# Kernel optimization log

Hardware: AMD Instinct MI355X
Metric: run time of the kernel (lower is better)

The kernel has to match this reference:

```python
import jax, jax.numpy as jnp
import numpy as np

ALPHA = 300.0  # attractor strength (exp variant: exp(-alpha*|dx|^gamma)*dx, gamma=2)


def setup_inputs() -> dict:
    key = jax.random.key(0)
    k0, k1, k2, k3 = jax.random.split(key, 4)
    n, c, h, w = 4, 256, 128, 128
    mlp_dim, n_attractors, n_bins = 128, 16, 64
    x = jax.random.normal(k0, (n, c, h, w), jnp.float32)
    b_prev = jax.random.uniform(k1, (n, n_bins, h, w), jnp.float32)  # bin centers
    w1 = jax.random.normal(k2, (mlp_dim, c), jnp.float32) * 0.02
    b1 = jnp.zeros((mlp_dim,), jnp.float32)
    w2 = jax.random.normal(k3, (n_attractors, mlp_dim), jnp.float32) * 0.02
    b2 = jnp.zeros((n_attractors,), jnp.float32)
    return {"x": x, "b_prev": b_prev, "w1": w1, "b1": b1, "w2": w2, "b2": b2}


def reference(x, b_prev, w1, b1, w2, b2):
    # 1x1 conv MLP head: Conv2d(c->mlp) -> ReLU -> Conv2d(mlp->n_attractors) -> Softplus
    hfeat = jax.nn.relu(jnp.einsum('nchw,oc->nohw', x, w1) + b1[None, :, None, None])
    A = jax.nn.softplus(jnp.einsum('nchw,oc->nohw', hfeat, w2) + b2[None, :, None, None])
    # b_prev interpolated to (h, w) == identity here (same spatial size)
    b_centers = b_prev
    # dx: [n, n_attractors, n_bins, h, w]
    dx = A[:, :, None, :, :] - b_centers[:, None, :, :, :]
    # exp attractor with gamma=2: exp(-alpha*dx^2) * dx, summed over attractors ('sum' kind)
    delta_c = jnp.sum(jnp.exp(-ALPHA * dx * dx) * dx, axis=1)
    b_new_centers = b_centers + delta_c
    return (b_new_centers, b_new_centers)
```

## Files before the change

### kernel.cpp

```cpp
#include <hip/hip_runtime.h>
#include <hip/hip_bf16.h>
#include <stdint.h>


#define HW 16384
#define ALPHA 300.0f

typedef short bf16x8_t __attribute__((ext_vector_type(8)));
typedef float f32x4_t __attribute__((ext_vector_type(4)));
typedef unsigned int u32x4_t __attribute__((ext_vector_type(4)));

__device__ __forceinline__ unsigned short f2bf(float f) {
  unsigned int u = __builtin_bit_cast(unsigned int, f);
  u += 0x7fffu + ((u >> 16) & 1u);
  return (unsigned short)(u >> 16);
}
__device__ __forceinline__ unsigned int pack2(float a, float b) {
  return (unsigned int)f2bf(a) | ((unsigned int)f2bf(b) << 16);
}

__global__ void zoed_prep(const float* __restrict__ w1,
                          const float* __restrict__ w2,
                          unsigned short* __restrict__ blob) {
  int i = blockIdx.x * 256 + threadIdx.x;
  if (i < 32768) {
    int o = i >> 8, c = i & 255;
    float v = w1[i];
    int idx = (c >> 5) * 4096 + o * 32 + ((((c >> 3) & 3) ^ (o & 3)) << 3) + (c & 7);
    blob[idx] = f2bf(v);
  } else {
    int i2 = i - 32768;
    int a = i2 >> 7, o = i2 & 127;
    float v = w2[i2];
    int idx = 32768 + (o >> 5) * 512 + a * 32 + ((((o >> 3) & 3) ^ (a & 3)) << 3) + (o & 7);
    blob[idx] = f2bf(v);
  }
}

__global__ __launch_bounds__(256, 4) void zoed_fused(
    const float* __restrict__ x, const float* __restrict__ bprev,
    const float* __restrict__ b1, const float* __restrict__ b2,
    const unsigned short* __restrict__ wblob, float* __restrict__ out) {
  __shared__ __align__(16) char smem[21504];

  const int t = threadIdx.x;
  const int lane = t & 63;
  const int l15 = lane & 15;
  const int quad = lane >> 4;
  const int wv = t >> 6;
  const int sw = ((quad ^ (l15 & 3)) << 4);

  const int blk = blockIdx.x;
  const int n = blk >> 8;
  const int p0 = ((blk & 255) << 6) + wv * 16;

  char* hid = smem + wv * 4096;
  char* Ab = smem + 16384 + wv * 1280;

  const float* xb = x + (size_t)(n * 256 + quad * 8) * HW + p0 + l15;

  float xr[4][8];
#pragma unroll
  for (int c = 0; c < 3; c++)
#pragma unroll
    for (int j = 0; j < 8; j++)
      xr[c][j] = xb[(size_t)(c * 32 + j) * HW];

  size_t obase = (size_t)(n * 64 + quad * 16) * HW + p0 + l15;
  const float* bp = bprev + obase;
  float bpr[16];

  f32x4_t acc[8];
#pragma unroll
  for (int i = 0; i < 8; i++) acc[i] = (f32x4_t){0.f, 0.f, 0.f, 0.f};

  const char* wb = (const char*)wblob + l15 * 64 + sw;

#pragma unroll
  for (int kb = 0; kb < 8; ++kb) {
    bf16x8_t af[8];
#pragma unroll
    for (int tm = 0; tm < 8; tm++)
      af[tm] = *(const bf16x8_t*)(wb + kb * 8192 + tm * 1024);
    if (kb < 5) {
#pragma unroll
      for (int j = 0; j < 8; j++)
        xr[(kb + 3) & 3][j] = xb[(size_t)((kb + 3) * 32 + j) * HW];
    }
    if (kb == 5) {
#pragma unroll
      for (int b = 0; b < 8; b++) bpr[b] = bp[(size_t)b * HW];
    }
    if (kb == 6) {
#pragma unroll
      for (int b = 8; b < 16; b++) bpr[b] = bp[(size_t)b * HW];
    }
    u32x4_t v = {pack2(xr[kb & 3][0], xr[kb & 3][1]),
                 pack2(xr[kb & 3][2], xr[kb & 3][3]),
                 pack2(xr[kb & 3][4], xr[kb & 3][5]),
                 pack2(xr[kb & 3][6], xr[kb & 3][7])};
    bf16x8_t bfm = __builtin_bit_cast(bf16x8_t, v);
#pragma unroll
    for (int tm = 0; tm < 8; tm++)
      acc[tm] = __builtin_amdgcn_mfma_f32_16x16x32_bf16(af[tm], bfm, acc[tm],
                                                        0, 0, 0);
  }

  bf16x8_t a2[4];
#pragma unroll
  for (int kc = 0; kc < 4; kc++)
    a2[kc] = *(const bf16x8_t*)((const char*)wblob + 65536 + kc * 1024 +
                                l15 * 64 + sw);

#pragma unroll
  for (int tm = 0; tm < 8; tm++) {
    f32x4_t b1v = *(const f32x4_t*)(b1 + tm * 16 + quad * 4);
    f32x4_t h = acc[tm] + b1v;
    h[0] = fmaxf(h[0], 0.f);
    h[1] = fmaxf(h[1], 0.f);
    h[2] = fmaxf(h[2], 0.f);
    h[3] = fmaxf(h[3], 0.f);
    int kc = tm >> 1;
    int g = (tm & 1) * 2 + (quad >> 1);
    int off8 = (quad & 1) * 8;
    unsigned int* dst = (unsigned int*)(hid + kc * 1024 + l15 * 64 +
                                        ((g ^ (l15 & 3)) << 4) + off8);
    dst[0] = pack2(h[0], h[1]);
    dst[1] = pack2(h[2], h[3]);
  }
  f32x4_t acc2 = (f32x4_t){0.f, 0.f, 0.f, 0.f};
#pragma unroll
  for (int kc = 0; kc < 4; kc++) {
    bf16x8_t bh = *(const bf16x8_t*)(hid + kc * 1024 + l15 * 64 + sw);
    acc2 = __builtin_amdgcn_mfma_f32_16x16x32_bf16(a2[kc], bh, acc2, 0, 0, 0);
  }
  {
    f32x4_t b2v = *(const f32x4_t*)(b2 + quad * 4);
    f32x4_t z = acc2 + b2v;
    f32x4_t spv;
#pragma unroll
    for (int r = 0; r < 4; r++) {
      float zz = z[r];
      spv[r] = fmaxf(zz, 0.f) + log1pf(__expf(-fabsf(zz)));
    }
    *(f32x4_t*)(Ab + l15 * 80 + quad * 16) = spv;
  }
  float Av[16];
#pragma unroll
  for (int r = 0; r < 4; r++) {
    f32x4_t v = *(const f32x4_t*)(Ab + l15 * 80 + r * 16);
    Av[r * 4 + 0] = v[0];
    Av[r * 4 + 1] = v[1];
    Av[r * 4 + 2] = v[2];
    Av[r * 4 + 3] = v[3];
  }
  float* o1 = out + obase;
  float* o2 = o1 + (size_t)256 * HW;
#pragma unroll
  for (int b = 0; b < 16; b++) {
    float c = bpr[b];
    float d0 = 0.f, d1 = 0.f;
#pragma unroll
    for (int a = 0; a < 8; a++) {
      float dx = Av[a] - c;
      float e = __expf(dx * dx * -ALPHA);
      d0 = fmaf(e, dx, d0);
    }
#pragma unroll
    for (int a = 8; a < 16; a++) {
      float dx = Av[a] - c;
      float e = __expf(dx * dx * -ALPHA);
      d1 = fmaf(e, dx, d1);
    }
    float r = c + (d0 + d1);
    __builtin_nontemporal_store(r, o1 + (size_t)b * HW);
    __builtin_nontemporal_store(r, o2 + (size_t)b * HW);
  }
}

extern "C" void kernel_launch(void* const* d_in, const int* in_sizes, int n_in,
                              void* d_out, int out_size, void* d_ws,
                              size_t ws_size, hipStream_t stream) {
  const float* x = (const float*)d_in[0];
  const float* bprev = (const float*)d_in[1];
  const float* w1 = (const float*)d_in[2];
  const float* b1 = (const float*)d_in[3];
  const float* w2 = (const float*)d_in[4];
  const float* b2 = (const float*)d_in[5];
  float* outp = (float*)d_out;
  unsigned short* blob = (unsigned short*)d_ws;

  zoed_prep<<<136, 256, 0, stream>>>(w1, w2, blob);
  zoed_fused<<<1024, 256, 0, stream>>>(x, bprev, b1, b2, blob, outp);
}
```

Measured before the change: 145.8 us.

## Software-pipeline weight and input loads with inline asm and explicit vmcnt waits

The first GEMM loop is unrolled by hand into a macro. It double-buffers the weight fragments and issues the x loads through inline-asm global loads, with explicit s_waitcnt vmcnt counts and sched barriers, so that memory latency overlaps the MFMAs in a controlled way. The bprev loads move after the GEMM instead of being interleaved with it, and launch bounds drop from 4 to 3 blocks per CU to leave room for more registers. The risks are lower occupancy, the bprev load latency now being exposed, and fragile hand-counted vmcnt values.

Result: faster. 140.9 us (-3.3%).

```diff
diff --git a/kernel.cpp b/kernel.cpp
--- a/kernel.cpp
+++ b/kernel.cpp
@@ -17,6 +17,16 @@
 }
 __device__ __forceinline__ unsigned int pack2(float a, float b) {
   return (unsigned int)f2bf(a) | ((unsigned int)f2bf(b) << 16);
+}
+__device__ __forceinline__ float ald(const float* p) {
+  float r;
+  asm volatile("global_load_dword %0, %1, off" : "=v"(r) : "v"(p));
+  return r;
+}
+__device__ __forceinline__ u32x4_t ald4(const void* p) {
+  u32x4_t r;
+  asm volatile("global_load_dwordx4 %0, %1, off" : "=v"(r) : "v"(p));
+  return r;
 }
 
 __global__ void zoed_prep(const float* __restrict__ w1,
@@ -37,7 +47,31 @@
   }
 }
 
-__global__ __launch_bounds__(256, 4) void zoed_fused(
+#define KITER(KB, NWAIT, AFNEXT, XNEXT)                                     \
+  {                                                                         \
+    constexpr int kb = KB;                                                  \
+    if (AFNEXT) {                                                           \
+      _Pragma("unroll") for (int tm = 0; tm < 8; tm++)                      \
+          af[(kb + 1) & 1][tm] = ald4(wb + (kb + 1) * 8192 + tm * 1024);    \
+    }                                                                       \
+    if (XNEXT) {                                                            \
+      _Pragma("unroll") for (int j = 0; j < 8; j++)                         \
+          xr[(kb + 3) & 3][j] = ald(xb + (size_t)((kb + 3) * 32 + j) * HW); \
+    }                                                                       \
+    asm volatile("s_waitcnt vmcnt(" #NWAIT ")");                            \
+    __builtin_amdgcn_sched_barrier(0);                                      \
+    u32x4_t v = {pack2(xr[kb & 3][0], xr[kb & 3][1]),                       \
+                 pack2(xr[kb & 3][2], xr[kb & 3][3]),                       \
+                 pack2(xr[kb & 3][4], xr[kb & 3][5]),                       \
+                 pack2(xr[kb & 3][6], xr[kb & 3][7])};                      \
+    bf16x8_t bfm = __builtin_bit_cast(bf16x8_t, v);                         \
+    _Pragma("unroll") for (int tm = 0; tm < 8; tm++)                        \
+        acc[tm] = __builtin_amdgcn_mfma_f32_16x16x32_bf16(                  \
+            __builtin_bit_cast(bf16x8_t, af[kb & 1][tm]), bfm, acc[tm], 0,  \
+            0, 0);                                                          \
+  }
+
+__global__ __launch_bounds__(256, 3) void zoed_fused(
     const float* __restrict__ x, const float* __restrict__ bprev,
     const float* __restrict__ b1, const float* __restrict__ b2,
     const unsigned short* __restrict__ wblob, float* __restrict__ out) {
@@ -58,54 +92,36 @@
   char* Ab = smem + 16384 + wv * 1280;
 
   const float* xb = x + (size_t)(n * 256 + quad * 8) * HW + p0 + l15;
-
+  const char* wb = (const char*)wblob + l15 * 64 + sw;
+
+  u32x4_t af[2][8];
+#pragma unroll
+  for (int tm = 0; tm < 8; tm++) af[0][tm] = ald4(wb + tm * 1024);
   float xr[4][8];
 #pragma unroll
   for (int c = 0; c < 3; c++)
 #pragma unroll
     for (int j = 0; j < 8; j++)
-      xr[c][j] = xb[(size_t)(c * 32 + j) * HW];
+      xr[c][j] = ald(xb + (size_t)(c * 32 + j) * HW);
+
+  f32x4_t acc[8];
+#pragma unroll
+  for (int i = 0; i < 8; i++) acc[i] = (f32x4_t){0.f, 0.f, 0.f, 0.f};
+
+  KITER(0, 32, 1, 1)
+  KITER(1, 24, 1, 1)
+  KITER(2, 24, 1, 1)
+  KITER(3, 24, 1, 1)
+  KITER(4, 24, 1, 1)
+  KITER(5, 16, 1, 0)
+  KITER(6, 8, 1, 0)
+  KITER(7, 0, 0, 0)
 
   size_t obase = (size_t)(n * 64 + quad * 16) * HW + p0 + l15;
   const float* bp = bprev + obase;
   float bpr[16];
-
-  f32x4_t acc[8];
-#pragma unroll
-  for (int i = 0; i < 8; i++) acc[i] = (f32x4_t){0.f, 0.f, 0.f, 0.f};
-
-  const char* wb = (const char*)wblob + l15 * 64 + sw;
-
-#pragma unroll
-  for (int kb = 0; kb < 8; ++kb) {
-    bf16x8_t af[8];
-#pragma unroll
-    for (int tm = 0; tm < 8; tm++)
-      af[tm] = *(const bf16x8_t*)(wb + kb * 8192 + tm * 1024);
-    if (kb < 5) {
-#pragma unroll
-      for (int j = 0; j < 8; j++)
-        xr[(kb + 3) & 3][j] = xb[(size_t)((kb + 3) * 32 + j) * HW];
-    }
-    if (kb == 5) {
-#pragma unroll
-      for (int b = 0; b < 8; b++) bpr[b] = bp[(size_t)b * HW];
-    }
-    if (kb == 6) {
-#pragma unroll
-      for (int b = 8; b < 16; b++) bpr[b] = bp[(size_t)b * HW];
-    }
-    u32x4_t v = {pack2(xr[kb & 3][0], xr[kb & 3][1]),
-                 pack2(xr[kb & 3][2], xr[kb & 3][3]),
-                 pack2(xr[kb & 3][4], xr[kb & 3][5]),
-                 pack2(xr[kb & 3][6], xr[kb & 3][7])};
-    bf16x8_t bfm = __builtin_bit_cast(bf16x8_t, v);
-#pragma unroll
-    for (int tm = 0; tm < 8; tm++)
-      acc[tm] = __builtin_amdgcn_mfma_f32_16x16x32_bf16(af[tm], bfm, acc[tm],
-                                                        0, 0, 0);
-  }
-
+#pragma unroll
+  for (int b = 0; b < 16; b++) bpr[b] = bp[(size_t)b * HW];
   bf16x8_t a2[4];
 #pragma unroll
   for (int kc = 0; kc < 4; kc++)
```
